# Kernel optimization log

Measured on AMD Instinct MI355X. Metric: run time of the kernel, lower is better.

## Reference

```python
import jax, jax.numpy as jnp
import numpy as np
import math

NEG_INF = -1e9  # stand-in for Const.NegInf
D_QKV = 64

def setup_inputs() -> dict:
    key = jax.random.key(0)
    kq, kk, kv, km = jax.random.split(key, 4)
    B, H, S, D = 4, 16, 2048, D_QKV
    q = jax.random.normal(kq, (B, H, S, D), dtype=jnp.float32)
    k = jax.random.normal(kk, (B, H, S, D), dtype=jnp.float32)
    v = jax.random.normal(kv, (B, H, S, D), dtype=jnp.float32)
    mask = jax.random.randint(km, (1, 1, S, S), 0, 2, dtype=jnp.int32)
    return {"q": q, "k": k, "v": v, "mask": mask, "batch": B, "q_seq": S}

def reference(q, k, v, mask, batch, q_seq):
    # scores: (B, H, Sq, Sk)
    scores = jnp.einsum('bhqd,bhkd->bhqk', q, k) / math.sqrt(D_QKV)
    # NOTE: non-standard order (faithful to source): log_softmax FIRST,
    # (dropout skipped since dropout_rate == 0), THEN post-softmax masking.
    score = jax.nn.log_softmax(scores, axis=-1)
    score = jnp.where(mask == 0, jnp.asarray(NEG_INF, score.dtype), score)
    att = jnp.einsum('bhqk,bhkd->bhqd', score, v)
    # (B, H, Sq, D) -> (B, Sq, H*D)
    return att.transpose(0, 2, 1, 3).reshape(batch, q_seq, -1)
```

## Files before the change

### kernel.cpp

```cpp
#include <hip/hip_runtime.h>

#define S_LEN 2048

typedef __attribute__((ext_vector_type(8))) short bf16x8;
typedef __attribute__((ext_vector_type(4))) float f32x4;
typedef __attribute__((ext_vector_type(4))) unsigned int u32x4;
typedef unsigned long long u64;
typedef unsigned int u32;
typedef unsigned short u16;

#define MFMA16 __builtin_amdgcn_mfma_f32_16x16x32_bf16

__device__ __forceinline__ u32 asu(float f) { union { float f; u32 u; } v; v.f = f; return v.u; }

__device__ __forceinline__ u32 pkbf(float a, float b) {
  return __builtin_amdgcn_perm(asu(b) + 0x8000u, asu(a) + 0x8000u, 0x07060302u);
}

__device__ __forceinline__ u64* qkaddr(u16* dst, int row, int c4) {
  const int cb = c4 >> 1;
  return (u64*)((char*)dst + ((((row << 3) + (cb ^ (row & 7))) << 4) + ((c4 & 1) << 3)));
}
__device__ __forceinline__ bf16x8 ldfrag(const u16* base, int row, int blk) {
  const char* p = (const char*)base + (((row << 3) + (blk ^ (row & 7))) << 4);
  return *(const bf16x8*)p;
}

__device__ __forceinline__ void gload16(const u16* g, u16* l) {
  __builtin_amdgcn_global_load_lds((const __attribute__((address_space(1))) void*)g,
                                   (__attribute__((address_space(3))) void*)l, 16, 0, 0);
}

__global__ __launch_bounds__(256) void prep_kernel(
    const float* __restrict__ gk, const float* __restrict__ gv,
    const int* __restrict__ gmask,
    u16* __restrict__ wsK, u16* __restrict__ wsV,
    u16* __restrict__ wsM, float* __restrict__ wsVs) {
  __shared__ float red[256];
  const int bid = blockIdx.x, t = threadIdx.x;
  if (bid < 2048) {
    const int bh = bid >> 5, kt = bid & 31;
    const float* kg = gk + ((size_t)bh << 17) + ((size_t)kt << 12);
    const float* vg = gv + ((size_t)bh << 17) + ((size_t)kt << 12);
    u16* outK = wsK + ((size_t)bid << 12);
    u16* outV = wsV + ((size_t)bid << 12);
#pragma unroll
    for (int i = 0; i < 2; ++i) {
      const int n = t + (i << 8);
      const int row = n >> 3, cb = (n & 7) ^ (row & 7);
      {
        const float4 A = *(const float4*)(kg + (row << 6) + (cb << 3));
        const float4 B = *(const float4*)(kg + (row << 6) + (cb << 3) + 4);
        u32x4 w;
        w.x = pkbf(A.x, A.y); w.y = pkbf(A.z, A.w);
        w.z = pkbf(B.x, B.y); w.w = pkbf(B.z, B.w);
        *(u32x4*)(outK + ((size_t)n << 3)) = w;
      }
      {
        float e[8];
#pragma unroll
        for (int j = 0; j < 8; ++j) e[j] = vg[(((cb << 3) + j) << 6) + row];
        u32x4 w;
        w.x = pkbf(e[0], e[1]); w.y = pkbf(e[2], e[3]);
        w.z = pkbf(e[4], e[5]); w.w = pkbf(e[6], e[7]);
        *(u32x4*)(outV + ((size_t)n << 3)) = w;
      }
    }
  } else if (bid < 3072) {
    const size_t base = ((size_t)(bid - 2048) << 12) + ((size_t)t << 4);
    int4 m[4];
#pragma unroll
    for (int i = 0; i < 4; ++i) m[i] = *(const int4*)(gmask + base + (i << 2));
    u32x4 w0, w1;
    w0.x = (m[0].x ? 0xFFFFu : 0u) | (m[0].y ? 0xFFFF0000u : 0u);
    w0.y = (m[0].z ? 0xFFFFu : 0u) | (m[0].w ? 0xFFFF0000u : 0u);
    w0.z = (m[1].x ? 0xFFFFu : 0u) | (m[1].y ? 0xFFFF0000u : 0u);
    w0.w = (m[1].z ? 0xFFFFu : 0u) | (m[1].w ? 0xFFFF0000u : 0u);
    w1.x = (m[2].x ? 0xFFFFu : 0u) | (m[2].y ? 0xFFFF0000u : 0u);
    w1.y = (m[2].z ? 0xFFFFu : 0u) | (m[2].w ? 0xFFFF0000u : 0u);
    w1.z = (m[3].x ? 0xFFFFu : 0u) | (m[3].y ? 0xFFFF0000u : 0u);
    w1.w = (m[3].z ? 0xFFFFu : 0u) | (m[3].w ? 0xFFFF0000u : 0u);
    *(u32x4*)(wsM + base) = w0;
    *(u32x4*)(wsM + base + 8) = w1;
  } else {
    const int bh = bid - 3072;
    const float* vg = gv + ((size_t)bh << 17);
    const int d = t & 63, sl = t >> 6;
    const int k0 = sl << 9;
    float s = 0.f;
#pragma unroll 8
    for (int k = 0; k < 512; ++k) s += vg[((size_t)(k0 + k) << 6) + d];
    red[t] = s;
    __syncthreads();
    if (t < 64)
      wsVs[(bh << 6) + t] = (red[t] + red[t + 64]) + (red[t + 128] + red[t + 192]);
  }
}

__global__ __launch_bounds__(256, 4) void attn_kernel(
    const float* __restrict__ gq, const u16* __restrict__ wsK,
    const u16* __restrict__ wsV, const u16* __restrict__ wsM,
    const float* __restrict__ wsVs, float* __restrict__ gout) {
  __shared__ __align__(16) u16 sK[2][4096];
  __shared__ __align__(16) u16 sV[2][4096];
  __shared__ __align__(16) u16 sW1[4096];

  const int t = threadIdx.x;
  const int wv = t >> 6;
  const int lane = t & 63;
  const int c = lane & 15;
  const int quad = lane >> 4;
  const int r0 = t >> 4, c4 = t & 15;

  const int bx = blockIdx.x;
  const int bh = bx & 63;
  const int q0 = (bx >> 6) << 6;

  const float* qg = gq + ((size_t)bh << 17) + ((size_t)q0 << 6);
  const u16* srcK = wsK + ((size_t)bh << 17) + (t << 3);
  const u16* srcV = wsV + ((size_t)bh << 17) + (t << 3);
  const int qrow = q0 + (wv << 4) + c;
  const u16* mrow = wsM + ((size_t)qrow << 11) + (quad << 3);

  f32x4 vreg[4];
#pragma unroll
  for (int mt = 0; mt < 4; ++mt)
    vreg[mt] = *(const f32x4*)(wsVs + (bh << 6) + (mt << 4) + (quad << 2));

  const float qs = 0.1803368801111204f;
#pragma unroll
  for (int i = 0; i < 4; ++i) {
    const int row = r0 + (i << 4);
    const float4 f = *(const float4*)(qg + ((size_t)row << 6) + (c4 << 2));
    const u32 lo = pkbf(f.x * qs, f.y * qs);
    const u32 hi = pkbf(f.z * qs, f.w * qs);
    *qkaddr(sW1, row, c4) = (u64)lo | ((u64)hi << 32);
  }
  __syncthreads();
  bf16x8 qf[2];
#pragma unroll
  for (int ks = 0; ks < 2; ++ks)
    qf[ks] = ldfrag(sW1, (wv << 4) + c, (ks << 2) + quad);
  asm volatile("s_waitcnt lgkmcnt(0)" ::: "memory");

  f32x4 accA[4], accB[4];
#pragma unroll
  for (int mt = 0; mt < 4; ++mt) {
    const f32x4 z = {0.f, 0.f, 0.f, 0.f};
    accA[mt] = z; accB[mt] = z;
  }
  float lacc = 0.f;

#define STAGE(kt_, buf_) do {                                        \
    const u16* sk_ = srcK + ((kt_) << 12);                           \
    const u16* sv_ = srcV + ((kt_) << 12);                           \
    u16* dk_ = &sK[buf_][wv << 9];                                   \
    u16* dv_ = &sV[buf_][wv << 9];                                   \
    gload16(sk_, dk_);                                               \
    gload16(sk_ + 2048, dk_ + 2048);                                 \
    gload16(sv_, dv_);                                               \
    gload16(sv_ + 2048, dv_ + 2048);                                 \
  } while (0)

  STAGE(0, 0);

  for (int kt = 0; kt < 32; ++kt) {
    const int cur = kt & 1;
    const u16* sKc = sK[cur];
    const u16* sVc = sV[cur];
    const u32x4 mm0 = *(const u32x4*)(mrow + ((size_t)kt << 6));
    const u32x4 mm1 = *(const u32x4*)(mrow + ((size_t)kt << 6) + 32);
    if (kt < 31) {
      STAGE(kt + 1, cur ^ 1);
      asm volatile("s_waitcnt vmcnt(6)" ::: "memory");
    } else {
      asm volatile("s_waitcnt vmcnt(2)" ::: "memory");
    }
    __builtin_amdgcn_s_barrier();
    asm volatile("" ::: "memory");

#pragma unroll
    for (int tr = 0; tr < 4; ++tr) {
      f32x4 acc = {0.f, 0.f, 0.f, 0.f};
      acc = MFMA16(ldfrag(sKc, (tr << 4) + c, quad), qf[0], acc, 0, 0, 0);
      acc = MFMA16(ldfrag(sKc, (tr << 4) + c, 4 + quad), qf[1], acc, 0, 0, 0);
      lacc += (exp2f(acc[0]) + exp2f(acc[1])) + (exp2f(acc[2]) + exp2f(acc[3]));
      *qkaddr(sW1, (wv << 4) + c, (tr << 2) + quad) =
          (u64)pkbf(acc[0], acc[1]) | ((u64)pkbf(acc[2], acc[3]) << 32);
    }
#pragma unroll
    for (int ks = 0; ks < 2; ++ks) {
      const u32x4 m = ks ? mm1 : mm0;
      const bf16x8 wr = ldfrag(sW1, (wv << 4) + c, (ks << 2) + quad);
      const u32x4 wraw = __builtin_bit_cast(u32x4, wr);
      const bf16x8 bw1 = __builtin_bit_cast(bf16x8, wraw & m);
      const bf16x8 bw2 = __builtin_bit_cast(bf16x8, m & 0x3F803F80u);
#pragma unroll
      for (int mt = 0; mt < 4; ++mt) {
        const bf16x8 av = ldfrag(sVc, (mt << 4) + c, (ks << 2) + quad);
        accA[mt] = MFMA16(av, bw1, accA[mt], 0, 0, 0);
        accB[mt] = MFMA16(av, bw2, accB[mt], 0, 0, 0);
      }
    }
    asm volatile("s_waitcnt lgkmcnt(0)" ::: "memory");
    __builtin_amdgcn_s_barrier();
  }
#undef STAGE

  float l = lacc;
  l += __shfl_xor(l, 16, 64);
  l += __shfl_xor(l, 32, 64);
  l = __log2f(l) * 0.6931471805599453f;
  const float c1 = 1e9f - l;

  const int b = bh >> 4, h = bh & 15;
  const float ln2 = 0.6931471805599453f;
#pragma unroll
  for (int mt = 0; mt < 4; ++mt) {
    float4 o;
    o.x = ln2 * accA[mt][0] + c1 * accB[mt][0] - 1e9f * vreg[mt][0];
    o.y = ln2 * accA[mt][1] + c1 * accB[mt][1] - 1e9f * vreg[mt][1];
    o.z = ln2 * accA[mt][2] + c1 * accB[mt][2] - 1e9f * vreg[mt][2];
    o.w = ln2 * accA[mt][3] + c1 * accB[mt][3] - 1e9f * vreg[mt][3];
    const size_t off = ((size_t)b * S_LEN + (size_t)qrow) * 1024 +
                       (h << 6) + (mt << 4) + (quad << 2);
    *(float4*)(gout + off) = o;
  }
}

extern "C" void kernel_launch(void* const* d_in, const int* in_sizes, int n_in,
                              void* d_out, int out_size, void* d_ws, size_t ws_size,
                              hipStream_t stream) {
  const float* q = (const float*)d_in[0];
  const float* k = (const float*)d_in[1];
  const float* v = (const float*)d_in[2];
  const int* mask = (const int*)d_in[3];
  (void)in_sizes; (void)n_in; (void)out_size; (void)ws_size;
  u16* wsK = (u16*)d_ws;
  u16* wsV = wsK + ((size_t)64 << 17);
  u16* wsM = wsV + ((size_t)64 << 17);
  float* wsVs = (float*)(wsM + ((size_t)S_LEN * S_LEN));
  prep_kernel<<<dim3(3136), dim3(256), 0, stream>>>(k, v, mask, wsK, wsV, wsM, wsVs);
  attn_kernel<<<dim3(2048), dim3(256), 0, stream>>>(q, wsK, wsV, wsM, wsVs, (float*)d_out);
}
```

Baseline: 334.2 us.

## Transpose V via LDS, fuse V column sums with atomics, use hardware cvt/exp

The prep kernel now loads V tiles coalesced into a padded LDS tile and transposes them there, instead of doing strided global gathers. The per-column V sums are computed from the same tile and accumulated with atomicAdd, which removes the separate 64 column-sum blocks but needs a memset before launch. Separately, the manual rounding bf16 pack is replaced by v_cvt_pk_bf16_f32 and exp2f by raw v_exp_f32 in both kernels. This trims conversion and exp instruction count in the attention inner loop, at the risk of small differences in rounding and denormal handling.

```diff
diff --git a/kernel.cpp b/kernel.cpp
--- a/kernel.cpp
+++ b/kernel.cpp
@@ -11,10 +11,15 @@
 
 #define MFMA16 __builtin_amdgcn_mfma_f32_16x16x32_bf16
 
-__device__ __forceinline__ u32 asu(float f) { union { float f; u32 u; } v; v.f = f; return v.u; }
-
-__device__ __forceinline__ u32 pkbf(float a, float b) {
-  return __builtin_amdgcn_perm(asu(b) + 0x8000u, asu(a) + 0x8000u, 0x07060302u);
+__device__ __forceinline__ u32 cvtpk(float a, float b) {
+  u32 r;
+  asm("v_cvt_pk_bf16_f32 %0, %1, %2" : "=v"(r) : "v"(a), "v"(b));
+  return r;
+}
+__device__ __forceinline__ float exp2hw(float x) {
+  float r;
+  asm("v_exp_f32 %0, %1" : "=v"(r) : "v"(x));
+  return r;
 }
 
 __device__ __forceinline__ u64* qkaddr(u16* dst, int row, int c4) {
@@ -36,7 +41,8 @@
     const int* __restrict__ gmask,
     u16* __restrict__ wsK, u16* __restrict__ wsV,
     u16* __restrict__ wsM, float* __restrict__ wsVs) {
-  __shared__ float red[256];
+  __shared__ float tile[64 * 65];
+  __shared__ float sred[2][256];
   const int bid = blockIdx.x, t = threadIdx.x;
   if (bid < 2048) {
     const int bh = bid >> 5, kt = bid & 31;
@@ -44,29 +50,51 @@
     const float* vg = gv + ((size_t)bh << 17) + ((size_t)kt << 12);
     u16* outK = wsK + ((size_t)bid << 12);
     u16* outV = wsV + ((size_t)bid << 12);
+    const int r0 = t >> 4, c4 = t & 15;
+#pragma unroll
+    for (int i = 0; i < 4; ++i) {
+      const int row = r0 + (i << 4);
+      const float4 f = *(const float4*)(vg + (row << 6) + (c4 << 2));
+      float* p = tile + row;
+      p[((c4 << 2) + 0) * 65] = f.x;
+      p[((c4 << 2) + 1) * 65] = f.y;
+      p[((c4 << 2) + 2) * 65] = f.z;
+      p[((c4 << 2) + 3) * 65] = f.w;
+    }
 #pragma unroll
     for (int i = 0; i < 2; ++i) {
       const int n = t + (i << 8);
       const int row = n >> 3, cb = (n & 7) ^ (row & 7);
-      {
-        const float4 A = *(const float4*)(kg + (row << 6) + (cb << 3));
-        const float4 B = *(const float4*)(kg + (row << 6) + (cb << 3) + 4);
-        u32x4 w;
-        w.x = pkbf(A.x, A.y); w.y = pkbf(A.z, A.w);
-        w.z = pkbf(B.x, B.y); w.w = pkbf(B.z, B.w);
-        *(u32x4*)(outK + ((size_t)n << 3)) = w;
-      }
-      {
-        float e[8];
-#pragma unroll
-        for (int j = 0; j < 8; ++j) e[j] = vg[(((cb << 3) + j) << 6) + row];
-        u32x4 w;
-        w.x = pkbf(e[0], e[1]); w.y = pkbf(e[2], e[3]);
-        w.z = pkbf(e[4], e[5]); w.w = pkbf(e[6], e[7]);
-        *(u32x4*)(outV + ((size_t)n << 3)) = w;
-      }
-    }
-  } else if (bid < 3072) {
+      const float4 A = *(const float4*)(kg + (row << 6) + (cb << 3));
+      const float4 B = *(const float4*)(kg + (row << 6) + (cb << 3) + 4);
+      u32x4 w;
+      w.x = cvtpk(A.x, A.y); w.y = cvtpk(A.z, A.w);
+      w.z = cvtpk(B.x, B.y); w.w = cvtpk(B.z, B.w);
+      *(u32x4*)(outK + ((size_t)n << 3)) = w;
+    }
+    __syncthreads();
+#pragma unroll
+    for (int i = 0; i < 2; ++i) {
+      const int n = t + (i << 8);
+      const int d = n >> 3, cb = (n & 7) ^ (d & 7);
+      const float* src = tile + d * 65 + (cb << 3);
+      float e[8], s = 0.f;
+#pragma unroll
+      for (int j = 0; j < 8; ++j) { e[j] = src[j]; s += e[j]; }
+      sred[i][t] = s;
+      u32x4 w;
+      w.x = cvtpk(e[0], e[1]); w.y = cvtpk(e[2], e[3]);
+      w.z = cvtpk(e[4], e[5]); w.w = cvtpk(e[6], e[7]);
+      *(u32x4*)(outV + ((size_t)n << 3)) = w;
+    }
+    __syncthreads();
+    if (t < 64) {
+      const float* s8 = (t < 32) ? &sred[0][t << 3] : &sred[1][(t - 32) << 3];
+      const float s = ((s8[0] + s8[1]) + (s8[2] + s8[3])) +
+                      ((s8[4] + s8[5]) + (s8[6] + s8[7]));
+      atomicAdd(&wsVs[(bh << 6) + t], s);
+    }
+  } else {
     const size_t base = ((size_t)(bid - 2048) << 12) + ((size_t)t << 4);
     int4 m[4];
 #pragma unroll
@@ -82,18 +110,6 @@
     w1.w = (m[3].z ? 0xFFFFu : 0u) | (m[3].w ? 0xFFFF0000u : 0u);
     *(u32x4*)(wsM + base) = w0;
     *(u32x4*)(wsM + base + 8) = w1;
-  } else {
-    const int bh = bid - 3072;
-    const float* vg = gv + ((size_t)bh << 17);
-    const int d = t & 63, sl = t >> 6;
-    const int k0 = sl << 9;
-    float s = 0.f;
-#pragma unroll 8
-    for (int k = 0; k < 512; ++k) s += vg[((size_t)(k0 + k) << 6) + d];
-    red[t] = s;
-    __syncthreads();
-    if (t < 64)
-      wsVs[(bh << 6) + t] = (red[t] + red[t + 64]) + (red[t + 128] + red[t + 192]);
   }
 }
 
@@ -132,8 +148,8 @@
   for (int i = 0; i < 4; ++i) {
     const int row = r0 + (i << 4);
     const float4 f = *(const float4*)(qg + ((size_t)row << 6) + (c4 << 2));
-    const u32 lo = pkbf(f.x * qs, f.y * qs);
-    const u32 hi = pkbf(f.z * qs, f.w * qs);
+    const u32 lo = cvtpk(f.x * qs, f.y * qs);
+    const u32 hi = cvtpk(f.z * qs, f.w * qs);
     *qkaddr(sW1, row, c4) = (u64)lo | ((u64)hi << 32);
   }
   __syncthreads();
@@ -184,9 +200,9 @@
       f32x4 acc = {0.f, 0.f, 0.f, 0.f};
       acc = MFMA16(ldfrag(sKc, (tr << 4) + c, quad), qf[0], acc, 0, 0, 0);
       acc = MFMA16(ldfrag(sKc, (tr << 4) + c, 4 + quad), qf[1], acc, 0, 0, 0);
-      lacc += (exp2f(acc[0]) + exp2f(acc[1])) + (exp2f(acc[2]) + exp2f(acc[3]));
+      lacc += (exp2hw(acc[0]) + exp2hw(acc[1])) + (exp2hw(acc[2]) + exp2hw(acc[3]));
       *qkaddr(sW1, (wv << 4) + c, (tr << 2) + quad) =
-          (u64)pkbf(acc[0], acc[1]) | ((u64)pkbf(acc[2], acc[3]) << 32);
+          (u64)cvtpk(acc[0], acc[1]) | ((u64)cvtpk(acc[2], acc[3]) << 32);
     }
 #pragma unroll
     for (int ks = 0; ks < 2; ++ks) {
@@ -240,6 +256,7 @@
   u16* wsV = wsK + ((size_t)64 << 17);
   u16* wsM = wsV + ((size_t)64 << 17);
   float* wsVs = (float*)(wsM + ((size_t)S_LEN * S_LEN));
-  prep_kernel<<<dim3(3136), dim3(256), 0, stream>>>(k, v, mask, wsK, wsV, wsM, wsVs);
+  hipMemsetAsync(wsVs, 0, 64 * 64 * sizeof(float), stream);
+  prep_kernel<<<dim3(3072), dim3(256), 0, stream>>>(k, v, mask, wsK, wsV, wsM, wsVs);
   attn_kernel<<<dim3(2048), dim3(256), 0, stream>>>(q, wsK, wsV, wsM, wsVs, (float*)d_out);
 }
```

Result: faster. 295.5 us (-11.6%).
